# Optimization experiments

Measured on AMD Instinct MI355X. Metric: run time of the kernel, lower is better.

## Reference

```python
import jax, jax.numpy as jnp
import numpy as np

LENGTH_SCALE = 0.1


def setup_inputs() -> dict:
    key = jax.random.key(0)
    k1, k2, k3 = jax.random.split(key, 3)
    features = jax.random.normal(k1, (8, 512, 128, 128), dtype=jnp.float32)
    # nn.Parameter init: normal(0, 0.05)
    weights = jax.random.normal(k2, (16, 64, 512), dtype=jnp.float32) * 0.05
    m = jax.random.normal(k3, (16, 64), dtype=jnp.float32)
    N = jnp.ones((64,), dtype=jnp.float32) * 12.0  # buffer init: ones * 12
    return {"features": features, "weights": weights, "m": m, "N": N}


def reference(features, weights, m, N):
    # per-class linear embedding projection: [b,f,h,w] x [e,c,f] -> [b,e,c,h,w]
    embeddings = jnp.einsum('bfhw,ecf->bechw', features, weights)
    centroids = m / N  # [e, c]
    gamma = -1.0 / (2.0 * LENGTH_SCALE ** 2)
    diff = embeddings - centroids[None, :, :, None, None]
    # squared L2, mean over embedding dim e, RBF exp -> [b, c, h, w]
    out = jnp.exp(jnp.mean(diff * diff, axis=1) * gamma)
    return out
```

## Files before the change

kernel.cpp:

```cpp
#include <hip/hip_runtime.h>

typedef __attribute__((ext_vector_type(8))) short bf16x8;
typedef __attribute__((ext_vector_type(4))) float f32x4;
typedef __attribute__((ext_vector_type(4))) float f4;
typedef __attribute__((ext_vector_type(2))) unsigned int u32x2;
typedef __attribute__((ext_vector_type(4))) unsigned int u32x4;

#define HW   16384
#define FDIM 512

__device__ __forceinline__ unsigned pkhi(float a, float b) {
    return __builtin_amdgcn_perm(__builtin_bit_cast(unsigned int, b),
                                 __builtin_bit_cast(unsigned int, a),
                                 0x07060302u);
}
__device__ __forceinline__ float trhi(float a) {
    return __builtin_bit_cast(float, __builtin_bit_cast(unsigned int, a) & 0xFFFF0000u);
}
__device__ __forceinline__ unsigned pklo(float a, float b) {
    return pkhi(a - trhi(a), b - trhi(b));
}

__global__ __launch_bounds__(256) void conv_w(const float* __restrict__ wts,
                                              unsigned short* __restrict__ wh,
                                              unsigned short* __restrict__ wl) {
    const int tid = blockIdx.x * 256 + threadIdx.x;
    const int n  = tid & 1023;
    const int kc = tid >> 10;
    const float* src = wts + (size_t)((n & 15) * 64 + (n >> 4)) * FDIM + kc * 8;
    f4 a = *(const f4*)src, b = *(const f4*)(src + 4);
    u32x4 h = { pkhi(a[0], a[1]), pkhi(a[2], a[3]), pkhi(b[0], b[1]), pkhi(b[2], b[3]) };
    u32x4 l = { pklo(a[0], a[1]), pklo(a[2], a[3]), pklo(b[0], b[1]), pklo(b[2], b[3]) };
    size_t off = ((size_t)kc * 1024 + n) * 8;
    *(u32x4*)(wh + off) = h;
    *(u32x4*)(wl + off) = l;
}

__global__ __launch_bounds__(256, 4) void duq_main(
    const float* __restrict__ feat,
    const unsigned short* __restrict__ wh,
    const unsigned short* __restrict__ wl,
    const float* __restrict__ m_in,
    const float* __restrict__ n_in,
    float* __restrict__ out)
{
    __shared__ __align__(16) unsigned short Ah[128 * 40];
    __shared__ __align__(16) unsigned short Al[128 * 40];

    const int t  = threadIdx.x;
    const int bx = blockIdx.x;
    const int nb = bx & 7;
    const int mb = bx >> 3;
    const int bidx = mb >> 7;
    const int hw0  = (mb & 127) << 7;

    const int fb = t & 7;
    const int pb = t >> 3;
    const float* ap = feat + (size_t)bidx * (FDIM * HW) + (size_t)(fb * 4) * HW + (hw0 + pb * 4);
    unsigned short* awH = &Ah[(pb * 4) * 40 + fb * 4];
    unsigned short* awL = &Al[(pb * 4) * 40 + fb * 4];

    const int lane = t & 63;
    const int wv = t >> 6;
    const int wm = wv >> 1, wn = wv & 1;
    const int l16 = lane & 15, qd = lane >> 4;

    const unsigned short* arH = &Ah[(wm * 64 + l16) * 40 + qd * 8];
    const unsigned short* arL = &Al[(wm * 64 + l16) * 40 + qd * 8];

    const size_t bgoff = ((size_t)qd * 1024 + (size_t)(nb * 128 + wn * 64 + l16)) * 8;
    const unsigned short* bgh = wh + bgoff;
    const unsigned short* bgl = wl + bgoff;

    f32x4 acc[4][4] = {};

    f4 av[4];
    #pragma unroll
    for (int i = 0; i < 4; ++i) av[i] = *(const f4*)(ap + (size_t)i * HW);

    bf16x8 cbh = *(const bf16x8*)(bgh);
    bf16x8 cbl = *(const bf16x8*)(bgl);
    size_t boff = 0;

    for (int kt = 0; kt < 16; ++kt) {
        __syncthreads();
        #pragma unroll
        for (int j = 0; j < 4; ++j) {
            float a0 = av[0][j], a1 = av[1][j], a2 = av[2][j], a3 = av[3][j];
            u32x2 h, l;
            h[0] = pkhi(a0, a1); h[1] = pkhi(a2, a3);
            l[0] = pklo(a0, a1); l[1] = pklo(a2, a3);
            *(u32x2*)(awH + j * 40) = h;
            *(u32x2*)(awL + j * 40) = l;
        }
        __syncthreads();

        if (kt < 15) {
            ap += 32 * HW;
            #pragma unroll
            for (int i = 0; i < 4; ++i) av[i] = *(const f4*)(ap + (size_t)i * HW);
        }

        bf16x8 fah[4], fal[4];
        #pragma unroll
        for (int i = 0; i < 4; ++i) {
            fah[i] = *(const bf16x8*)(arH + i * 640);
            fal[i] = *(const bf16x8*)(arL + i * 640);
        }

        #pragma unroll
        for (int j = 0; j < 4; ++j) {
            size_t bnext = boff + ((j == 3) ? (size_t)(32768 - 384) : (size_t)128);
            bf16x8 nbh = *(const bf16x8*)(bgh + bnext);
            bf16x8 nbl = *(const bf16x8*)(bgl + bnext);
            #pragma unroll
            for (int i = 0; i < 4; ++i) {
                acc[i][j] = __builtin_amdgcn_mfma_f32_16x16x32_bf16(fah[i], cbh, acc[i][j], 0, 0, 0);
                acc[i][j] = __builtin_amdgcn_mfma_f32_16x16x32_bf16(fah[i], cbl, acc[i][j], 0, 0, 0);
                acc[i][j] = __builtin_amdgcn_mfma_f32_16x16x32_bf16(fal[i], cbh, acc[i][j], 0, 0, 0);
            }
            cbh = nbh; cbl = nbl; boff = bnext;
        }
    }

    float centv[4];
    #pragma unroll
    for (int j = 0; j < 4; ++j) {
        int cj = nb * 8 + wn * 4 + j;
        centv[j] = m_in[l16 * 64 + cj] / n_in[cj];
    }
    #pragma unroll
    for (int i = 0; i < 4; ++i) {
        #pragma unroll
        for (int j = 0; j < 4; ++j) {
            float s0 = acc[i][j][0] - centv[j]; s0 *= s0;
            float s1 = acc[i][j][1] - centv[j]; s1 *= s1;
            float s2 = acc[i][j][2] - centv[j]; s2 *= s2;
            float s3 = acc[i][j][3] - centv[j]; s3 *= s3;
            #pragma unroll
            for (int msk = 1; msk < 16; msk <<= 1) {
                s0 += __shfl_xor(s0, msk, 64);
                s1 += __shfl_xor(s1, msk, 64);
                s2 += __shfl_xor(s2, msk, 64);
                s3 += __shfl_xor(s3, msk, 64);
            }
            if (l16 == 0) {
                int cj = nb * 8 + wn * 4 + j;
                f4 o;
                o[0] = __expf(s0 * -3.125f);
                o[1] = __expf(s1 * -3.125f);
                o[2] = __expf(s2 * -3.125f);
                o[3] = __expf(s3 * -3.125f);
                size_t off = ((size_t)(bidx * 64 + cj)) * HW
                           + (size_t)(hw0 + wm * 64 + i * 16 + qd * 4);
                *(f4*)(out + off) = o;
            }
        }
    }
}

__global__ __launch_bounds__(256) void duq_fallback(
    const float* __restrict__ feat, const float* __restrict__ wts,
    const float* __restrict__ m_in, const float* __restrict__ n_in,
    float* __restrict__ out)
{
    __shared__ __align__(16) unsigned short Ah[128 * 40];
    __shared__ __align__(16) unsigned short Al[128 * 40];
    __shared__ __align__(16) unsigned short Bh[128 * 40];
    __shared__ __align__(16) unsigned short Bl[128 * 40];

    const int t  = threadIdx.x;
    const int bx = blockIdx.x;
    const int nb = bx & 7;
    const int mb = bx >> 3;
    const int bidx = mb >> 7;
    const int hw0  = (mb & 127) << 7;

    const int fb = t & 7;
    const int pb = t >> 3;
    const float* ap = feat + (size_t)bidx * (FDIM * HW) + (size_t)(fb * 4) * HW + (hw0 + pb * 4);

    const int bn  = t >> 1;
    const int bh_ = t & 1;
    const int ng  = nb * 128 + bn;
    const float* bp = wts + (size_t)((ng & 15) * 64 + (ng >> 4)) * FDIM + bh_ * 16;

    unsigned short* awH = &Ah[(pb * 4) * 40 + fb * 4];
    unsigned short* awL = &Al[(pb * 4) * 40 + fb * 4];
    unsigned short* bwH = &Bh[bn * 40 + bh_ * 16];
    unsigned short* bwL = &Bl[bn * 40 + bh_ * 16];

    const int lane = t & 63;
    const int wv = t >> 6;
    const int wm = wv >> 1, wn = wv & 1;
    const int l16 = lane & 15, qd = lane >> 4;

    const unsigned short* arH = &Ah[(wm * 64 + l16) * 40 + qd * 8];
    const unsigned short* arL = &Al[(wm * 64 + l16) * 40 + qd * 8];
    const unsigned short* brH = &Bh[(wn * 64 + l16) * 40 + qd * 8];
    const unsigned short* brL = &Bl[(wn * 64 + l16) * 40 + qd * 8];

    f32x4 acc[4][4] = {};

    f4 av[4], bv[4];
    #pragma unroll
    for (int i = 0; i < 4; ++i) av[i] = *(const f4*)(ap + (size_t)i * HW);
    #pragma unroll
    for (int q = 0; q < 4; ++q) bv[q] = *(const f4*)(bp + q * 4);

    for (int kt = 0; kt < 16; ++kt) {
        __syncthreads();
        #pragma unroll
        for (int j = 0; j < 4; ++j) {
            float a0 = av[0][j], a1 = av[1][j], a2 = av[2][j], a3 = av[3][j];
            u32x2 h, l;
            h[0] = pkhi(a0, a1); h[1] = pkhi(a2, a3);
            l[0] = pklo(a0, a1); l[1] = pklo(a2, a3);
            *(u32x2*)(awH + j * 40) = h;
            *(u32x2*)(awL + j * 40) = l;
        }
        {
            u32x4 h0 = { pkhi(bv[0][0], bv[0][1]), pkhi(bv[0][2], bv[0][3]),
                         pkhi(bv[1][0], bv[1][1]), pkhi(bv[1][2], bv[1][3]) };
            u32x4 h1 = { pkhi(bv[2][0], bv[2][1]), pkhi(bv[2][2], bv[2][3]),
                         pkhi(bv[3][0], bv[3][1]), pkhi(bv[3][2], bv[3][3]) };
            u32x4 l0 = { pklo(bv[0][0], bv[0][1]), pklo(bv[0][2], bv[0][3]),
                         pklo(bv[1][0], bv[1][1]), pklo(bv[1][2], bv[1][3]) };
            u32x4 l1 = { pklo(bv[2][0], bv[2][1]), pklo(bv[2][2], bv[2][3]),
                         pklo(bv[3][0], bv[3][1]), pklo(bv[3][2], bv[3][3]) };
            *(u32x4*)(bwH)     = h0;  *(u32x4*)(bwH + 8) = h1;
            *(u32x4*)(bwL)     = l0;  *(u32x4*)(bwL + 8) = l1;
        }
        __syncthreads();

        if (kt < 15) {
            ap += 32 * HW;
            bp += 32;
            #pragma unroll
            for (int i = 0; i < 4; ++i) av[i] = *(const f4*)(ap + (size_t)i * HW);
            #pragma unroll
            for (int q = 0; q < 4; ++q) bv[q] = *(const f4*)(bp + q * 4);
        }

        bf16x8 fah[4], fal[4];
        #pragma unroll
        for (int i = 0; i < 4; ++i) {
            fah[i] = *(const bf16x8*)(arH + i * 640);
            fal[i] = *(const bf16x8*)(arL + i * 640);
        }
        #pragma unroll
        for (int j = 0; j < 4; ++j) {
            bf16x8 fbh = *(const bf16x8*)(brH + j * 640);
            bf16x8 fbl = *(const bf16x8*)(brL + j * 640);
            #pragma unroll
            for (int i = 0; i < 4; ++i) {
                acc[i][j] = __builtin_amdgcn_mfma_f32_16x16x32_bf16(fah[i], fbh, acc[i][j], 0, 0, 0);
                acc[i][j] = __builtin_amdgcn_mfma_f32_16x16x32_bf16(fah[i], fbl, acc[i][j], 0, 0, 0);
                acc[i][j] = __builtin_amdgcn_mfma_f32_16x16x32_bf16(fal[i], fbh, acc[i][j], 0, 0, 0);
            }
        }
    }

    float centv[4];
    #pragma unroll
    for (int j = 0; j < 4; ++j) {
        int cj = nb * 8 + wn * 4 + j;
        centv[j] = m_in[l16 * 64 + cj] / n_in[cj];
    }
    #pragma unroll
    for (int i = 0; i < 4; ++i) {
        #pragma unroll
        for (int j = 0; j < 4; ++j) {
            float s0 = acc[i][j][0] - centv[j]; s0 *= s0;
            float s1 = acc[i][j][1] - centv[j]; s1 *= s1;
            float s2 = acc[i][j][2] - centv[j]; s2 *= s2;
            float s3 = acc[i][j][3] - centv[j]; s3 *= s3;
            #pragma unroll
            for (int msk = 1; msk < 16; msk <<= 1) {
                s0 += __shfl_xor(s0, msk, 64);
                s1 += __shfl_xor(s1, msk, 64);
                s2 += __shfl_xor(s2, msk, 64);
                s3 += __shfl_xor(s3, msk, 64);
            }
            if (l16 == 0) {
                int cj = nb * 8 + wn * 4 + j;
                f4 o;
                o[0] = __expf(s0 * -3.125f);
                o[1] = __expf(s1 * -3.125f);
                o[2] = __expf(s2 * -3.125f);
                o[3] = __expf(s3 * -3.125f);
                size_t off = ((size_t)(bidx * 64 + cj)) * HW
                           + (size_t)(hw0 + wm * 64 + i * 16 + qd * 4);
                *(f4*)(out + off) = o;
            }
        }
    }
}

extern "C" void kernel_launch(void* const* d_in, const int* in_sizes, int n_in,
                              void* d_out, int out_size, void* d_ws, size_t ws_size,
                              hipStream_t stream) {
    const float* feat = (const float*)d_in[0];
    const float* wts  = (const float*)d_in[1];
    const float* mbuf = (const float*)d_in[2];
    const float* nbuf = (const float*)d_in[3];
    float* out = (float*)d_out;

    if (ws_size >= (size_t)(2 * 1024 * 1024 + 128 * 1024)) {
        unsigned short* wh = (unsigned short*)d_ws;
        unsigned short* wl = wh + 512 * 1024;
        conv_w<<<dim3(256), dim3(256), 0, stream>>>(wts, wh, wl);
        duq_main<<<dim3(1024 * 8), dim3(256), 0, stream>>>(feat, wh, wl, mbuf, nbuf, out);
    } else {
        duq_fallback<<<dim3(1024 * 8), dim3(256), 0, stream>>>(feat, wts, mbuf, nbuf, out);
    }
}
```

Baseline: 726.5 us.

## Switch to 32x32x16 MFMA with double-buffered LDS and one barrier per k-step

The main kernel now uses 32x32x16 bf16 MFMA tiles instead of 16x16x32, which changes the fragment layout and the epilogue reduction. The A tile in LDS is double-buffered so that packing the next k-slice overlaps the MFMAs on the current one, and the two __syncthreads per iteration become a single custom waitcnt+barrier. The aim is to cut barrier stalls and fragment loads per FLOP. In exchange, LDS use doubles, the epilogue needs 16 shuffle reductions per cell, and the custom barrier relies on the waitcnt being correct.

After: 821.6 us. 13.1% more time.

```diff
diff --git a/kernel.cpp b/kernel.cpp
--- a/kernel.cpp
+++ b/kernel.cpp
@@ -1,6 +1,7 @@
 #include <hip/hip_runtime.h>
 
 typedef __attribute__((ext_vector_type(8))) short bf16x8;
+typedef __attribute__((ext_vector_type(16))) float f32x16;
 typedef __attribute__((ext_vector_type(4))) float f32x4;
 typedef __attribute__((ext_vector_type(4))) float f4;
 typedef __attribute__((ext_vector_type(2))) unsigned int u32x2;
@@ -8,6 +9,10 @@
 
 #define HW   16384
 #define FDIM 512
+#define LSTR 40
+#define LBUF 5120
+
+#define BARRIER() asm volatile("s_waitcnt lgkmcnt(0)\n\ts_barrier" ::: "memory")
 
 __device__ __forceinline__ unsigned pkhi(float a, float b) {
     return __builtin_amdgcn_perm(__builtin_bit_cast(unsigned int, b),
@@ -36,6 +41,26 @@
     *(u32x4*)(wl + off) = l;
 }
 
+__device__ __forceinline__ void packA(const f4* av, unsigned short* aH, unsigned short* aL) {
+    #pragma unroll
+    for (int j = 0; j < 4; ++j) {
+        float a0 = av[0][j], a1 = av[1][j], a2 = av[2][j], a3 = av[3][j];
+        u32x2 h, l;
+        h[0] = pkhi(a0, a1); h[1] = pkhi(a2, a3);
+        l[0] = pklo(a0, a1); l[1] = pklo(a2, a3);
+        *(u32x2*)(aH + j * LSTR) = h;
+        *(u32x2*)(aL + j * LSTR) = l;
+    }
+}
+
+#define MFMA_CELL(jn, FH, FL)                                                              \
+    acc[0][jn] = __builtin_amdgcn_mfma_f32_32x32x16_bf16(FH[0], cbh, acc[0][jn], 0, 0, 0); \
+    acc[1][jn] = __builtin_amdgcn_mfma_f32_32x32x16_bf16(FH[1], cbh, acc[1][jn], 0, 0, 0); \
+    acc[0][jn] = __builtin_amdgcn_mfma_f32_32x32x16_bf16(FH[0], cbl, acc[0][jn], 0, 0, 0); \
+    acc[1][jn] = __builtin_amdgcn_mfma_f32_32x32x16_bf16(FH[1], cbl, acc[1][jn], 0, 0, 0); \
+    acc[0][jn] = __builtin_amdgcn_mfma_f32_32x32x16_bf16(FL[0], cbh, acc[0][jn], 0, 0, 0); \
+    acc[1][jn] = __builtin_amdgcn_mfma_f32_32x32x16_bf16(FL[1], cbh, acc[1][jn], 0, 0, 0);
+
 __global__ __launch_bounds__(256, 4) void duq_main(
     const float* __restrict__ feat,
     const unsigned short* __restrict__ wh,
@@ -44,8 +69,8 @@
     const float* __restrict__ n_in,
     float* __restrict__ out)
 {
-    __shared__ __align__(16) unsigned short Ah[128 * 40];
-    __shared__ __align__(16) unsigned short Al[128 * 40];
+    __shared__ __align__(16) unsigned short Ah[2 * LBUF];
+    __shared__ __align__(16) unsigned short Al[2 * LBUF];
 
     const int t  = threadIdx.x;
     const int bx = blockIdx.x;
@@ -57,102 +82,106 @@
     const int fb = t & 7;
     const int pb = t >> 3;
     const float* ap = feat + (size_t)bidx * (FDIM * HW) + (size_t)(fb * 4) * HW + (hw0 + pb * 4);
-    unsigned short* awH = &Ah[(pb * 4) * 40 + fb * 4];
-    unsigned short* awL = &Al[(pb * 4) * 40 + fb * 4];
+    const int awo = (pb * 4) * LSTR + fb * 4;
 
     const int lane = t & 63;
     const int wv = t >> 6;
     const int wm = wv >> 1, wn = wv & 1;
-    const int l16 = lane & 15, qd = lane >> 4;
-
-    const unsigned short* arH = &Ah[(wm * 64 + l16) * 40 + qd * 8];
-    const unsigned short* arL = &Al[(wm * 64 + l16) * 40 + qd * 8];
-
-    const size_t bgoff = ((size_t)qd * 1024 + (size_t)(nb * 128 + wn * 64 + l16)) * 8;
-    const unsigned short* bgh = wh + bgoff;
-    const unsigned short* bgl = wl + bgoff;
-
-    f32x4 acc[4][4] = {};
+    const int lane32 = lane & 31;
+    const int khalf  = lane >> 5;
+
+    const int aro = (wm * 64 + lane32) * LSTR + khalf * 8;
+
+    const int n0 = nb * 128 + wn * 64 + lane32;
+    const size_t bo0 = ((size_t)khalf * 1024 + n0) * 8;
+    const unsigned short* bgh = wh + bo0;
+    const unsigned short* bgl = wl + bo0;
+
+    f32x16 acc[2][2] = {};
 
     f4 av[4];
     #pragma unroll
     for (int i = 0; i < 4; ++i) av[i] = *(const f4*)(ap + (size_t)i * HW);
-
     bf16x8 cbh = *(const bf16x8*)(bgh);
     bf16x8 cbl = *(const bf16x8*)(bgl);
-    size_t boff = 0;
+
+    packA(av, Ah + awo, Al + awo);
+    ap += 32 * HW;
+    #pragma unroll
+    for (int i = 0; i < 4; ++i) av[i] = *(const f4*)(ap + (size_t)i * HW);
+    BARRIER();
 
     for (int kt = 0; kt < 16; ++kt) {
-        __syncthreads();
-        #pragma unroll
-        for (int j = 0; j < 4; ++j) {
-            float a0 = av[0][j], a1 = av[1][j], a2 = av[2][j], a3 = av[3][j];
-            u32x2 h, l;
-            h[0] = pkhi(a0, a1); h[1] = pkhi(a2, a3);
-            l[0] = pklo(a0, a1); l[1] = pklo(a2, a3);
-            *(u32x2*)(awH + j * 40) = h;
-            *(u32x2*)(awL + j * 40) = l;
-        }
-        __syncthreads();
-
-        if (kt < 15) {
+        const int rb = (kt & 1) ? LBUF : 0;
+        const int wb = LBUF - rb;
+
+        bf16x8 fh0[2], fl0[2];
+        #pragma unroll
+        for (int im = 0; im < 2; ++im) {
+            fh0[im] = *(const bf16x8*)(&Ah[rb + aro + im * 1280]);
+            fl0[im] = *(const bf16x8*)(&Al[rb + aro + im * 1280]);
+        }
+        if (kt < 15) packA(av, Ah + wb + awo, Al + wb + awo);
+        if (kt < 14) {
             ap += 32 * HW;
             #pragma unroll
             for (int i = 0; i < 4; ++i) av[i] = *(const f4*)(ap + (size_t)i * HW);
         }
 
-        bf16x8 fah[4], fal[4];
-        #pragma unroll
-        for (int i = 0; i < 4; ++i) {
-            fah[i] = *(const bf16x8*)(arH + i * 640);
-            fal[i] = *(const bf16x8*)(arL + i * 640);
-        }
-
-        #pragma unroll
-        for (int j = 0; j < 4; ++j) {
-            size_t bnext = boff + ((j == 3) ? (size_t)(32768 - 384) : (size_t)128);
-            bf16x8 nbh = *(const bf16x8*)(bgh + bnext);
-            bf16x8 nbl = *(const bf16x8*)(bgl + bnext);
-            #pragma unroll
-            for (int i = 0; i < 4; ++i) {
-                acc[i][j] = __builtin_amdgcn_mfma_f32_16x16x32_bf16(fah[i], cbh, acc[i][j], 0, 0, 0);
-                acc[i][j] = __builtin_amdgcn_mfma_f32_16x16x32_bf16(fah[i], cbl, acc[i][j], 0, 0, 0);
-                acc[i][j] = __builtin_amdgcn_mfma_f32_16x16x32_bf16(fal[i], cbh, acc[i][j], 0, 0, 0);
-            }
-            cbh = nbh; cbl = nbl; boff = bnext;
-        }
-    }
-
-    float centv[4];
-    #pragma unroll
-    for (int j = 0; j < 4; ++j) {
-        int cj = nb * 8 + wn * 4 + j;
-        centv[j] = m_in[l16 * 64 + cj] / n_in[cj];
-    }
-    #pragma unroll
-    for (int i = 0; i < 4; ++i) {
-        #pragma unroll
-        for (int j = 0; j < 4; ++j) {
-            float s0 = acc[i][j][0] - centv[j]; s0 *= s0;
-            float s1 = acc[i][j][1] - centv[j]; s1 *= s1;
-            float s2 = acc[i][j][2] - centv[j]; s2 *= s2;
-            float s3 = acc[i][j][3] - centv[j]; s3 *= s3;
-            #pragma unroll
-            for (int msk = 1; msk < 16; msk <<= 1) {
-                s0 += __shfl_xor(s0, msk, 64);
-                s1 += __shfl_xor(s1, msk, 64);
-                s2 += __shfl_xor(s2, msk, 64);
-                s3 += __shfl_xor(s3, msk, 64);
-            }
-            if (l16 == 0) {
-                int cj = nb * 8 + wn * 4 + j;
+        const size_t kto = (size_t)kt * 32768;
+        bf16x8 nh = *(const bf16x8*)(bgh + kto + 256);
+        bf16x8 nl = *(const bf16x8*)(bgl + kto + 256);
+        MFMA_CELL(0, fh0, fl0);
+        cbh = nh; cbl = nl;
+        nh = *(const bf16x8*)(bgh + kto + 16384);
+        nl = *(const bf16x8*)(bgl + kto + 16384);
+        bf16x8 fh1[2], fl1[2];
+        #pragma unroll
+        for (int im = 0; im < 2; ++im) {
+            fh1[im] = *(const bf16x8*)(&Ah[rb + aro + im * 1280 + 16]);
+            fl1[im] = *(const bf16x8*)(&Al[rb + aro + im * 1280 + 16]);
+        }
+        MFMA_CELL(1, fh0, fl0);
+        cbh = nh; cbl = nl;
+        nh = *(const bf16x8*)(bgh + kto + 16640);
+        nl = *(const bf16x8*)(bgl + kto + 16640);
+        MFMA_CELL(0, fh1, fl1);
+        cbh = nh; cbl = nl;
+        nh = *(const bf16x8*)(bgh + kto + 32768);
+        nl = *(const bf16x8*)(bgl + kto + 32768);
+        MFMA_CELL(1, fh1, fl1);
+        cbh = nh; cbl = nl;
+
+        if (kt < 15) BARRIER();
+    }
+
+    const int l16  = lane & 15;
+    const int half = lane >> 5;
+    #pragma unroll
+    for (int im = 0; im < 2; ++im) {
+        #pragma unroll
+        for (int jn = 0; jn < 2; ++jn) {
+            const int c = nb * 8 + wn * 4 + jn * 2 + ((lane >> 4) & 1);
+            const float cent = m_in[l16 * 64 + c] / n_in[c];
+            float s[16];
+            #pragma unroll
+            for (int r = 0; r < 16; ++r) {
+                float d = acc[im][jn][r] - cent;
+                s[r] = d * d;
+            }
+            #pragma unroll
+            for (int r = 0; r < 16; ++r) {
+                #pragma unroll
+                for (int msk = 1; msk < 16; msk <<= 1)
+                    s[r] += __shfl_xor(s[r], msk, 64);
+            }
+            if (l16 < 4) {
+                const int q = l16;
                 f4 o;
-                o[0] = __expf(s0 * -3.125f);
-                o[1] = __expf(s1 * -3.125f);
-                o[2] = __expf(s2 * -3.125f);
-                o[3] = __expf(s3 * -3.125f);
-                size_t off = ((size_t)(bidx * 64 + cj)) * HW
-                           + (size_t)(hw0 + wm * 64 + i * 16 + qd * 4);
+                #pragma unroll
+                for (int z = 0; z < 4; ++z) o[z] = __expf(s[4 * q + z] * -3.125f);
+                size_t off = ((size_t)(bidx * 64 + c)) * HW
+                           + (size_t)(hw0 + wm * 64 + im * 32 + 8 * q + 4 * half);
                 *(f4*)(out + off) = o;
             }
         }
@@ -164,10 +193,10 @@
     const float* __restrict__ m_in, const float* __restrict__ n_in,
     float* __restrict__ out)
 {
-    __shared__ __align__(16) unsigned short Ah[128 * 40];
-    __shared__ __align__(16) unsigned short Al[128 * 40];
-    __shared__ __align__(16) unsigned short Bh[128 * 40];
-    __shared__ __align__(16) unsigned short Bl[128 * 40];
+    __shared__ __align__(16) unsigned short FAh[128 * 40];
+    __shared__ __align__(16) unsigned short FAl[128 * 40];
+    __shared__ __align__(16) unsigned short FBh[128 * 40];
+    __shared__ __align__(16) unsigned short FBl[128 * 40];
 
     const int t  = threadIdx.x;
     const int bx = blockIdx.x;
@@ -185,20 +214,20 @@
     const int ng  = nb * 128 + bn;
     const float* bp = wts + (size_t)((ng & 15) * 64 + (ng >> 4)) * FDIM + bh_ * 16;
 
-    unsigned short* awH = &Ah[(pb * 4) * 40 + fb * 4];
-    unsigned short* awL = &Al[(pb * 4) * 40 + fb * 4];
-    unsigned short* bwH = &Bh[bn * 40 + bh_ * 16];
-    unsigned short* bwL = &Bl[bn * 40 + bh_ * 16];
+    unsigned short* awH = &FAh[(pb * 4) * 40 + fb * 4];
+    unsigned short* awL = &FAl[(pb * 4) * 40 + fb * 4];
+    unsigned short* bwH = &FBh[bn * 40 + bh_ * 16];
+    unsigned short* bwL = &FBl[bn * 40 + bh_ * 16];
 
     const int lane = t & 63;
     const int wv = t >> 6;
     const int wm = wv >> 1, wn = wv & 1;
     const int l16 = lane & 15, qd = lane >> 4;
 
-    const unsigned short* arH = &Ah[(wm * 64 + l16) * 40 + qd * 8];
-    const unsigned short* arL = &Al[(wm * 64 + l16) * 40 + qd * 8];
-    const unsigned short* brH = &Bh[(wn * 64 + l16) * 40 + qd * 8];
-    const unsigned short* brL = &Bl[(wn * 64 + l16) * 40 + qd * 8];
+    const unsigned short* arH = &FAh[(wm * 64 + l16) * 40 + qd * 8];
+    const unsigned short* arL = &FAl[(wm * 64 + l16) * 40 + qd * 8];
+    const unsigned short* brH = &FBh[(wn * 64 + l16) * 40 + qd * 8];
+    const unsigned short* brL = &FBl[(wn * 64 + l16) * 40 + qd * 8];
 
     f32x4 acc[4][4] = {};
 
```
